# Kernel optimization log

Measured on AMD Instinct MI355X. Metric: run time of the kernel, lower is better.

## Reference

```python
import jax, jax.numpy as jnp
import numpy as np

K_SIZE = 3
STRIDE = 1
DIL = 1
PAD = (K_SIZE - 1) // 2 * DIL          # padding of the deformable conv
OFF_PAD = (K_SIZE - 1) // 2            # padding of the offset conv
KK = K_SIZE * K_SIZE


def setup_inputs() -> dict:
    key = jax.random.key(0)
    k1, k2, k3, k4 = jax.random.split(key, 4)
    B, C, H, W = 4, 256, 64, 64
    O = 256
    x = jax.random.normal(k1, (B, C, H, W), jnp.float32)
    # offset/mask conv params (small so sampled offsets stay in a realistic range)
    w_off = jax.random.normal(k2, (3 * KK, C, K_SIZE, K_SIZE), jnp.float32) * 0.01
    b_off = jax.random.normal(k3, (3 * KK,), jnp.float32) * 0.01
    # deformable conv weight (conv_dcn has bias=False in the source)
    w_dcn = jax.random.normal(k4, (O, C, K_SIZE, K_SIZE), jnp.float32) * (1.0 / np.sqrt(C * KK))
    return {"x": x, "w_off": w_off, "b_off": b_off, "w_dcn": w_dcn}


def _bilinear_sample(x, ys, xs):
    """x: [B,C,H,W]; ys, xs: [B,KK,Ho,Wo] fractional coords. Zero outside bounds.
    Returns [B,C,KK,Ho,Wo]."""
    B, C, H, W = x.shape
    _, K, Ho, Wo = ys.shape
    y0 = jnp.floor(ys)
    x0 = jnp.floor(xs)
    y1, x1 = y0 + 1.0, x0 + 1.0
    wy1 = ys - y0
    wy0 = 1.0 - wy1
    wx1 = xs - x0
    wx0 = 1.0 - wx1
    x_flat = x.reshape(B, C, H * W)

    def gather_term(yi, xi, wt):
        valid = (yi >= 0) & (yi < H) & (xi >= 0) & (xi < W)
        yc = jnp.clip(yi, 0, H - 1).astype(jnp.int32)
        xc = jnp.clip(xi, 0, W - 1).astype(jnp.int32)
        idx = (yc * W + xc).reshape(B, -1)                      # [B, K*Ho*Wo]
        g = jax.vmap(lambda xf, i: xf[:, i])(x_flat, idx)       # [B, C, K*Ho*Wo]
        w = (wt * valid.astype(wt.dtype)).reshape(B, 1, -1)
        return g * w

    out = (gather_term(y0, x0, wy0 * wx0)
           + gather_term(y0, x1, wy0 * wx1)
           + gather_term(y1, x0, wy1 * wx0)
           + gather_term(y1, x1, wy1 * wx1))
    return out.reshape(B, C, K, Ho, Wo)


def _dcn_v2(x, w_off, b_off, w_dcn):
    B, C, H, W = x.shape
    # offset/mask conv (standard conv, padding (k-1)//2)
    om = jax.lax.conv_general_dilated(
        x, w_off, (STRIDE, STRIDE), [(OFF_PAD, OFF_PAD)] * 2,
        dimension_numbers=("NCHW", "OIHW", "NCHW")) + b_off[None, :, None, None]
    offset = om[:, :2 * KK]                 # [B, 2*KK, Ho, Wo] as (dy0,dx0,dy1,dx1,...)
    mask = jax.nn.sigmoid(om[:, 2 * KK:])   # [B, KK, Ho, Wo]
    Ho, Wo = offset.shape[2], offset.shape[3]

    off = offset.reshape(B, KK, 2, Ho, Wo)
    off_y, off_x = off[:, :, 0], off[:, :, 1]

    kh = (jnp.arange(KK) // K_SIZE).astype(jnp.float32)
    kw = (jnp.arange(KK) % K_SIZE).astype(jnp.float32)
    py = (jnp.arange(Ho) * STRIDE - PAD).astype(jnp.float32)
    px = (jnp.arange(Wo) * STRIDE - PAD).astype(jnp.float32)

    ys = py[None, None, :, None] + (kh * DIL)[None, :, None, None] + off_y
    xs = px[None, None, None, :] + (kw * DIL)[None, :, None, None] + off_x

    sampled = _bilinear_sample(x, ys, xs)           # [B,C,KK,Ho,Wo]
    sampled = sampled * mask[:, None]               # modulated (DCNv2)
    w = w_dcn.reshape(w_dcn.shape[0], C, KK)
    return jnp.einsum("bckhw,ock->bohw", sampled, w)


def reference(x, w_off, b_off, w_dcn):
    return _dcn_v2(x, w_off, b_off, w_dcn)
```

## Files before the change

kernel.cpp:

```cpp
#include <hip/hip_runtime.h>

typedef __attribute__((ext_vector_type(8))) short short8;
typedef __attribute__((ext_vector_type(4))) float f32x4;

#define CIN 256
#define OUTC 256
#define HWW 4096
#define IMG_H 64
#define IMG_W 64
#define SROW 264
#define SB __builtin_amdgcn_sched_barrier(0)

__device__ __forceinline__ short f2bf(float f) {
    unsigned u = __float_as_uint(f);
    u += 0x7fffu + ((u >> 16) & 1u);
    return (short)(u >> 16);
}
__device__ __forceinline__ float bf2f(short s) {
    return __uint_as_float(((unsigned)(unsigned short)s) << 16);
}

__global__ __launch_bounds__(256) void prep(const float* __restrict__ x,
                                            const float* __restrict__ w_dcn,
                                            const float* __restrict__ w_off,
                                            short* __restrict__ xT,
                                            short* __restrict__ wF,
                                            short* __restrict__ wFo) {
    int bid = blockIdx.x;
    if (bid < 1024) {
        __shared__ float T[64][65];
        int p0 = (bid & 63) * 64;
        int c0 = ((bid >> 6) & 3) * 64;
        int b  = bid >> 8;
        int j = threadIdx.x & 63, i = threadIdx.x >> 6;
        const float* xb = x + ((size_t)b * CIN + c0) * HWW + p0;
#pragma unroll
        for (int k = 0; k < 16; ++k) {
            int row = i * 16 + k;
            T[row][j] = xb[(size_t)row * HWW + j];
        }
        __syncthreads();
        short* xTb = xT + ((size_t)b * HWW + p0) * CIN + c0;
#pragma unroll
        for (int k = 0; k < 16; ++k) {
            int prow = i * 16 + k;
            xTb[(size_t)prow * CIN + j] = f2bf(T[j][prow]);
        }
    } else if (bid < 1312) {
        int g = (bid - 1024) * 256 + threadIdx.x;
        int lane = g & 63;
        int rest = g >> 6;
        int octile = rest & 15;
        int step = rest >> 4;
        int kp = step >> 3, chv = step & 7;
        int oc = octile * 16 + (lane & 15);
        int cbase = chv * 32 + (lane >> 4) * 8;
        short8 v;
#pragma unroll
        for (int j = 0; j < 8; ++j)
            v[j] = f2bf(w_dcn[oc * 2304 + (cbase + j) * 9 + kp]);
        *(short8*)(wF + (size_t)g * 8) = v;
    } else {
        int g = (bid - 1312) * 256 + threadIdx.x;
        int lane = g & 63;
        int rest = g >> 6;
        int octile = rest & 1;
        int step = rest >> 1;
        int kp = step >> 3, chv = step & 7;
        int oc = octile * 16 + (lane & 15);
        int cbase = chv * 32 + (lane >> 4) * 8;
        short8 v;
#pragma unroll
        for (int j = 0; j < 8; ++j)
            v[j] = (oc < 27) ? f2bf(w_off[(oc * 256 + cbase + j) * 9 + kp]) : (short)0;
        *(short8*)(wFo + (size_t)g * 8) = v;
    }
}

__global__ __launch_bounds__(256) void offs_mfma(
        const short* __restrict__ xT, const short* __restrict__ wFo,
        float* __restrict__ P) {
    __shared__ short Sm[2][32 * SROW];

    int tid = threadIdx.x;
    int d = blockIdx.x;
    int L = (d & 7) * 64 + (d >> 3);
    int b = L >> 7;
    int ph = L & 127;
    int pbase = ph * 32;
    int prow = ph >> 1;
    int pc0 = (ph & 1) * 32;
    const short* xTb = xT + (size_t)b * HWW * CIN;

    int lane = tid & 63, wave = tid >> 6;
    int fr = lane & 15, fq = lane >> 4;
    int octile = wave & 1, pxt = wave >> 1;

    short8 st[4];

    auto loads = [&](int kp) {
        int yy = prow - 1 + kp / 3;
        int dx = kp % 3 - 1;
#pragma unroll
        for (int it = 0; it < 4; ++it) {
            int item = tid + it * 256;
            int cg8 = item & 31, px = item >> 5;
            int xx = pc0 + px + dx;
            bool ok = (yy >= 0 && yy < IMG_H && xx >= 0 && xx < IMG_W);
            int idx = ok ? ((yy * IMG_W + xx) * CIN + cg8 * 8) : 0;
            short8 v = *(const short8*)&xTb[idx];
            if (!ok) v = (short8){0,0,0,0,0,0,0,0};
            st[it] = v;
        }
    };
    auto writes = [&](int bufi) {
#pragma unroll
        for (int it = 0; it < 4; ++it) {
            int item = tid + it * 256;
            int cg8 = item & 31, px = item >> 5;
            *(short8*)&Sm[bufi][px * SROW + cg8 * 8] = st[it];
        }
    };

    f32x4 acc = (f32x4){0.f, 0.f, 0.f, 0.f};

    loads(0); writes(0);
    __syncthreads();
    for (int kp = 0; kp < 9; ++kp) {
        short8 aF[8];
#pragma unroll
        for (int chv = 0; chv < 8; ++chv)
            aF[chv] = *(const short8*)(wFo +
                    (((size_t)((kp * 8 + chv) * 2 + octile)) * 64 + lane) * 8);
        if (kp < 8) loads(kp + 1);
        const short* SmB = Sm[kp & 1];
#pragma unroll
        for (int chv = 0; chv < 8; ++chv) {
            short8 bF = *(const short8*)&SmB[(pxt * 16 + fr) * SROW + chv * 32 + fq * 8];
            acc = __builtin_amdgcn_mfma_f32_16x16x32_bf16(aF[chv], bF, acc, 0, 0, 0);
        }
        if (kp < 8) writes((kp + 1) & 1);
        __syncthreads();
    }

#pragma unroll
    for (int r = 0; r < 4; ++r) {
        int oc = octile * 16 + fq * 4 + r;
        if (oc < 27)
            P[((size_t)b * 32 + oc) * HWW + pbase + pxt * 16 + fr] = acc[r];
    }
}

__global__ __launch_bounds__(512) void dcn_main(
        const short* __restrict__ xT, const float* __restrict__ b_off,
        const float* __restrict__ P, const short* __restrict__ wF,
        float* __restrict__ out) {
    __shared__ short Sm[2][32 * 64 * 8];
    __shared__ float4 preW[576];
    __shared__ int4  preI[576];

    int tid = threadIdx.x;
    int d = blockIdx.x;
    int L = (d & 7) * 32 + (d >> 3);
    int b = L >> 6;
    int row = L & 63;
    int pbase = row * 64;
    const short* xTb = xT + (size_t)b * HWW * CIN;

    for (int e = tid; e < 576; e += 512) {
        int px = e & 63, kp = e >> 6;
        int p = pbase + px;
        float oy = P[((size_t)b * 32 + 2 * kp) * HWW + p] + b_off[2 * kp];
        float ox = P[((size_t)b * 32 + 2 * kp + 1) * HWW + p] + b_off[2 * kp + 1];
        float ml = P[((size_t)b * 32 + 18 + kp) * HWW + p] + b_off[18 + kp];
        float m = 1.0f / (1.0f + expf(-ml));
        float ys = (float)(row - 1 + kp / 3) + oy;
        float xs = (float)(px - 1 + kp % 3) + ox;
        float y0f = floorf(ys), x0f = floorf(xs);
        float fy = ys - y0f, fx = xs - x0f;
        int iy0 = (int)y0f, ix0 = (int)x0f;
        int iy1 = iy0 + 1, ix1 = ix0 + 1;
        float vy0 = (iy0 >= 0 && iy0 < IMG_H) ? 1.f : 0.f;
        float vy1 = (iy1 >= 0 && iy1 < IMG_H) ? 1.f : 0.f;
        float vx0 = (ix0 >= 0 && ix0 < IMG_W) ? 1.f : 0.f;
        float vx1 = (ix1 >= 0 && ix1 < IMG_W) ? 1.f : 0.f;
        int ry0 = min(max(iy0, 0), IMG_H - 1) * IMG_W;
        int ry1 = min(max(iy1, 0), IMG_H - 1) * IMG_W;
        int cx0 = min(max(ix0, 0), IMG_W - 1);
        int cx1 = min(max(ix1, 0), IMG_W - 1);
        float wy0 = 1.f - fy, wy1 = fy, wx0 = 1.f - fx, wx1 = fx;
        preW[e] = make_float4(wy0 * wx0 * vy0 * vx0 * m, wy0 * wx1 * vy0 * vx1 * m,
                              wy1 * wx0 * vy1 * vx0 * m, wy1 * wx1 * vy1 * vx1 * m);
        preI[e] = make_int4((ry0 + cx0) * CIN, (ry0 + cx1) * CIN,
                            (ry1 + cx0) * CIN, (ry1 + cx1) * CIN);
    }
    __syncthreads();

    int lane = tid & 63, wave = tid >> 6;
    int fr = lane & 15, fq = lane >> 4;
    int chunk = tid & 31, p0 = tid >> 5;
    int co = chunk * 8;

    auto soff = [](int s, int px) { return (s * 64 + (px & 32) + ((px & 31) ^ s)) * 8; };

    short8 stO[4][4];

    auto stage_loads = [&](int kq) {
#pragma unroll
        for (int it = 0; it < 4; ++it) {
            int px = p0 + it * 16;
            int4 iv = preI[kq * 64 + px];
            stO[it][0] = *(const short8*)&xTb[iv.x + co];
            stO[it][1] = *(const short8*)&xTb[iv.y + co];
            stO[it][2] = *(const short8*)&xTb[iv.z + co];
            stO[it][3] = *(const short8*)&xTb[iv.w + co];
        }
    };
    auto combine_writes = [&](int kq, int bufi) {
#pragma unroll
        for (int it = 0; it < 4; ++it) {
            int px = p0 + it * 16;
            float4 wv = preW[kq * 64 + px];
            short8 o;
#pragma unroll
            for (int j = 0; j < 8; ++j) {
                float v = wv.x * bf2f(stO[it][0][j]) + wv.y * bf2f(stO[it][1][j]) +
                          wv.z * bf2f(stO[it][2][j]) + wv.w * bf2f(stO[it][3][j]);
                o[j] = f2bf(v);
            }
            *(short8*)&Sm[bufi][soff(chunk, px)] = o;
        }
    };

    f32x4 acc[2][4];
#pragma unroll
    for (int m = 0; m < 2; ++m)
#pragma unroll
        for (int n = 0; n < 4; ++n)
            acc[m][n] = (f32x4){0.f, 0.f, 0.f, 0.f};

    stage_loads(0);
    SB;
    combine_writes(0, 0);
    __syncthreads();

#pragma unroll
    for (int kp = 0; kp < 9; ++kp) {
        short8 aFc[16];
#pragma unroll
        for (int chv = 0; chv < 8; ++chv)
#pragma unroll
            for (int m = 0; m < 2; ++m)
                aFc[chv * 2 + m] = *(const short8*)(wF +
                        (((size_t)((kp * 8 + chv) * 16 + wave * 2 + m)) * 64 + lane) * 8);
        SB;
        if (kp < 8) stage_loads(kp + 1);
        SB;
        {
            const short* SmB = Sm[kp & 1];
#pragma unroll
            for (int chv = 0; chv < 8; ++chv)
#pragma unroll
                for (int n = 0; n < 4; ++n) {
                    short8 bF = *(const short8*)&SmB[soff(chv * 4 + fq, n * 16 + fr)];
#pragma unroll
                    for (int m = 0; m < 2; ++m)
                        acc[m][n] = __builtin_amdgcn_mfma_f32_16x16x32_bf16(
                                aFc[chv * 2 + m], bF, acc[m][n], 0, 0, 0);
                }
        }
        SB;
        if (kp < 8) combine_writes(kp + 1, (kp + 1) & 1);
        __syncthreads();
    }

    float* outb = out + (size_t)b * (OUTC * HWW) + pbase;
#pragma unroll
    for (int m = 0; m < 2; ++m)
#pragma unroll
        for (int n = 0; n < 4; ++n)
#pragma unroll
            for (int r = 0; r < 4; ++r)
                outb[(size_t)(wave * 32 + m * 16 + fq * 4 + r) * HWW + n * 16 + fr] =
                        acc[m][n][r];
}

extern "C" void kernel_launch(void* const* d_in, const int* in_sizes, int n_in,
                              void* d_out, int out_size, void* d_ws, size_t ws_size,
                              hipStream_t stream) {
    const float* x     = (const float*)d_in[0];
    const float* w_off = (const float*)d_in[1];
    const float* b_off = (const float*)d_in[2];
    const float* w_dcn = (const float*)d_in[3];
    float* out = (float*)d_out;

    short* xT  = (short*)d_ws;
    float* P   = (float*)(xT + (size_t)4 * HWW * CIN);
    short* wF  = (short*)(P + (size_t)4 * 32 * HWW);
    short* wFo = wF + (size_t)73728 * 8;

    prep<<<1348, 256, 0, stream>>>(x, w_dcn, w_off, xT, wF, wFo);
    offs_mfma<<<512, 256, 0, stream>>>(xT, wFo, P);
    dcn_main<<<256, 512, 0, stream>>>(xT, b_off, P, wF, out);
}
```

Baseline: 62.21 us.

## Software-pipeline gather taps with inline asm loads and explicit vmcnt waits

Restructures the dcn_main main loop so that each iteration combines the taps already in flight into LDS, issues the next tap's gathers, and then runs the MFMAs. Gathers and weight fragments are issued with inline-asm global loads, and the code waits with explicit vmcnt counts so that the tap loads stay outstanding across the MFMA phase. The separate prologue combine is removed and the __syncthreads is replaced by an lgkmcnt wait plus s_barrier. Launch bounds now request 2 blocks per CU, which caps registers per thread. That cap risks spills given the large stO/aFc register arrays, and the hand-written waitcnt logic relies on the exact order in which loads are issued.

Result: faster. 58.54 us, median of 2 (-5.9%).

```diff
diff --git a/kernel.cpp b/kernel.cpp
--- a/kernel.cpp
+++ b/kernel.cpp
@@ -10,6 +10,10 @@
 #define IMG_W 64
 #define SROW 264
 #define SB __builtin_amdgcn_sched_barrier(0)
+#define GLOAD(dst, addr) \
+    asm volatile("global_load_dwordx4 %0, %1, off" : "=v"(dst) : "v"(addr) : "memory")
+#define WAITVM(n) asm volatile("s_waitcnt vmcnt(" #n ")" ::: "memory")
+#define WAITLGKM  asm volatile("s_waitcnt lgkmcnt(0)" ::: "memory")
 
 __device__ __forceinline__ short f2bf(float f) {
     unsigned u = __float_as_uint(f);
@@ -151,7 +155,7 @@
     }
 }
 
-__global__ __launch_bounds__(512) void dcn_main(
+__global__ __launch_bounds__(512, 2) void dcn_main(
         const short* __restrict__ xT, const float* __restrict__ b_off,
         const float* __restrict__ P, const short* __restrict__ wF,
         float* __restrict__ out) {
@@ -204,16 +208,17 @@
     auto soff = [](int s, int px) { return (s * 64 + (px & 32) + ((px & 31) ^ s)) * 8; };
 
     short8 stO[4][4];
-
-    auto stage_loads = [&](int kq) {
+    short8 aFc[16];
+
+    auto issue_taps = [&](int kq) {
 #pragma unroll
         for (int it = 0; it < 4; ++it) {
             int px = p0 + it * 16;
             int4 iv = preI[kq * 64 + px];
-            stO[it][0] = *(const short8*)&xTb[iv.x + co];
-            stO[it][1] = *(const short8*)&xTb[iv.y + co];
-            stO[it][2] = *(const short8*)&xTb[iv.z + co];
-            stO[it][3] = *(const short8*)&xTb[iv.w + co];
+            GLOAD(stO[it][0], (const short8*)&xTb[iv.x + co]);
+            GLOAD(stO[it][1], (const short8*)&xTb[iv.y + co]);
+            GLOAD(stO[it][2], (const short8*)&xTb[iv.z + co]);
+            GLOAD(stO[it][3], (const short8*)&xTb[iv.w + co]);
         }
     };
     auto combine_writes = [&](int kq, int bufi) {
@@ -239,25 +244,31 @@
         for (int n = 0; n < 4; ++n)
             acc[m][n] = (f32x4){0.f, 0.f, 0.f, 0.f};
 
-    stage_loads(0);
+    issue_taps(0);
     SB;
-    combine_writes(0, 0);
-    __syncthreads();
 
 #pragma unroll
     for (int kp = 0; kp < 9; ++kp) {
-        short8 aFc[16];
+        const int bufi = kp & 1;
 #pragma unroll
         for (int chv = 0; chv < 8; ++chv)
 #pragma unroll
             for (int m = 0; m < 2; ++m)
-                aFc[chv * 2 + m] = *(const short8*)(wF +
-                        (((size_t)((kp * 8 + chv) * 16 + wave * 2 + m)) * 64 + lane) * 8);
-        SB;
-        if (kp < 8) stage_loads(kp + 1);
+                GLOAD(aFc[chv * 2 + m], (const short8*)(wF +
+                        (((size_t)((kp * 8 + chv) * 16 + wave * 2 + m)) * 64 + lane) * 8));
+        SB;
+        WAITVM(16); SB;
+        combine_writes(kp, bufi);
+        SB;
+        if (kp < 8) issue_taps(kp + 1);
+        SB;
+        WAITLGKM;
+        __builtin_amdgcn_s_barrier();
+        SB;
+        if (kp < 8) { WAITVM(16); } else { WAITVM(0); }
         SB;
         {
-            const short* SmB = Sm[kp & 1];
+            const short* SmB = Sm[bufi];
 #pragma unroll
             for (int chv = 0; chv < 8; ++chv)
 #pragma unroll
@@ -270,8 +281,6 @@
                 }
         }
         SB;
-        if (kp < 8) combine_writes(kp + 1, (kp + 1) & 1);
-        __syncthreads();
     }
 
     float* outb = out + (size_t)b * (OUTC * HWW) + pbase;
```
